# Optimization experiments

Hardware: AMD Instinct MI355X
Metric: run time of the kernel (lower is better)

Reference implementation:

```python
import jax, jax.numpy as jnp
import numpy as np

N_NODES = 100000


def gcn_conv(x, edge_index, W, b):
    """PyG GCNConv: add self-loops, symmetric D^-1/2 (A+I) D^-1/2 normalization,
    linear transform, bias. Transform-then-aggregate (out_dim <= in_dim here)."""
    src, dst = edge_index[0], edge_index[1]
    h = x @ W  # [N, out]
    # degree including self-loop (edge_weight = 1)
    ones = jnp.ones(src.shape[0], dtype=x.dtype)
    deg = jax.ops.segment_sum(ones, dst, num_segments=N_NODES) + 1.0
    dinv = jax.lax.rsqrt(deg)  # [N]
    # normalized messages over real edges
    norm = dinv[src] * dinv[dst]  # [E]
    msgs = h[src] * norm[:, None]  # [E, out] -- dominant memory traffic
    agg = jax.ops.segment_sum(msgs, dst, num_segments=N_NODES)
    # self-loop contribution: norm_ii = dinv[i]^2
    agg = agg + h * (dinv * dinv)[:, None]
    return agg + b


def setup_inputs() -> dict:
    key = jax.random.key(0)
    k1, k2, k3, k4, k5, k6 = jax.random.split(key, 6)
    in_dim, hidden_dim, out_dim = 128, 64, 32
    n_edges = 1_600_000
    x = jax.random.normal(k1, (N_NODES, in_dim), dtype=jnp.float32)
    edge_index = jax.random.randint(k2, (2, n_edges), 0, N_NODES, dtype=jnp.int64)
    s1 = 1.0 / np.sqrt(in_dim)
    s2 = 1.0 / np.sqrt(hidden_dim)
    W1 = jax.random.uniform(k3, (in_dim, hidden_dim), jnp.float32, -s1, s1)
    b1 = jax.random.uniform(k4, (hidden_dim,), jnp.float32, -s1, s1)
    W2 = jax.random.uniform(k5, (hidden_dim, out_dim), jnp.float32, -s2, s2)
    b2 = jax.random.uniform(k6, (out_dim,), jnp.float32, -s2, s2)
    return {"x": x, "edge_index": edge_index, "W1": W1, "b1": b1, "W2": W2, "b2": b2}


def reference(x, edge_index, W1, b1, W2, b2):
    h = jax.nn.relu(gcn_conv(x, edge_index, W1, b1))
    return gcn_conv(h, edge_index, W2, b2)
```

## Files before the change

### kernel.cpp

```cpp
#include <hip/hip_runtime.h>

#define N_NODES 100000

__device__ __forceinline__ unsigned short f2bf_rn(float f) {
    unsigned int b = __float_as_uint(f);
    b += 0x7fffu + ((b >> 16) & 1u);
    return (unsigned short)(b >> 16);
}
__device__ __forceinline__ float bf_lo(unsigned int u) { return __uint_as_float(u << 16); }
__device__ __forceinline__ float bf_hi(unsigned int u) { return __uint_as_float(u & 0xffff0000u); }

__global__ __launch_bounds__(256) void bcount_kernel(const int* __restrict__ dst, int E,
                                                     unsigned int* __restrict__ bucket_totals) {
    __shared__ unsigned int cnt[256];
    int t = threadIdx.x;
    cnt[t] = 0;
    __syncthreads();
    int base = blockIdx.x * 4096;
#pragma unroll
    for (int k = 0; k < 16; ++k) {
        int e = base + k * 256 + t;
        if (e < E) {
            int d = __builtin_nontemporal_load(&dst[e]);
            atomicAdd(&cnt[(unsigned int)d >> 9], 1u);
        }
    }
    __syncthreads();
    if (cnt[t] > 0) atomicAdd(&bucket_totals[t], cnt[t]);
}

__global__ __launch_bounds__(256) void bscan_kernel(const unsigned int* __restrict__ totals,
                                                    int nb, int E,
                                                    unsigned int* __restrict__ bucket_base,
                                                    unsigned int* __restrict__ bucket_cursor) {
    __shared__ unsigned int s[256];
    int t = threadIdx.x;
    unsigned int v = (t < nb) ? totals[t] : 0u;
    s[t] = v; __syncthreads();
    for (int off = 1; off < 256; off <<= 1) {
        unsigned int x = s[t];
        unsigned int y = (t >= off) ? s[t - off] : 0u;
        __syncthreads();
        s[t] = x + y;
        __syncthreads();
    }
    if (t < nb) {
        unsigned int excl = s[t] - v;
        bucket_base[t] = excl;
        bucket_cursor[t] = excl;
    }
    if (t == 0) bucket_base[nb] = (unsigned int)E;
}

__global__ __launch_bounds__(256) void bin_kernel(const int* __restrict__ ei, int E,
                                                  unsigned int* __restrict__ bucket_cursor,
                                                  unsigned int* __restrict__ binned) {
    __shared__ unsigned int cnt[256];
    __shared__ unsigned int cur[256];
    int t = threadIdx.x;
    cnt[t] = 0;
    __syncthreads();
    int base = blockIdx.x * 4096;
    unsigned int pk[16];
    unsigned int bk[16];
#pragma unroll
    for (int k = 0; k < 16; ++k) {
        int e = base + k * 256 + t;
        if (e < E) {
            int s = __builtin_nontemporal_load(&ei[e]);
            int d = __builtin_nontemporal_load(&ei[E + e]);
            unsigned int b = (unsigned int)d >> 9;
            pk[k] = (unsigned int)s | (((unsigned int)d & 511u) << 17);
            bk[k] = b;
            atomicAdd(&cnt[b], 1u);
        } else {
            bk[k] = 0xFFFFFFFFu;
        }
    }
    __syncthreads();
    if (cnt[t] > 0) cur[t] = atomicAdd(&bucket_cursor[t], cnt[t]);
    __syncthreads();
#pragma unroll
    for (int k = 0; k < 16; ++k) {
        if (bk[k] != 0xFFFFFFFFu) {
            unsigned int pos = atomicAdd(&cur[bk[k]], 1u);
            binned[pos] = pk[k];
        }
    }
}

__global__ __launch_bounds__(512) void degb_kernel(const unsigned int* __restrict__ binned,
                                                   const unsigned int* __restrict__ bucket_base,
                                                   unsigned int* __restrict__ deg,
                                                   float* __restrict__ dinv, int N) {
    __shared__ unsigned int cnt[512];
    int t = threadIdx.x;
    cnt[t] = 0;
    int beg = (int)bucket_base[blockIdx.x];
    int end = (int)bucket_base[blockIdx.x + 1];
    __syncthreads();
    for (int i = beg + t; i < end; i += 512) {
        unsigned int u = __builtin_nontemporal_load(&binned[i]);
        atomicAdd(&cnt[u >> 17], 1u);
    }
    __syncthreads();
    int node = (blockIdx.x << 9) + t;
    if (node < N) {
        unsigned int c = cnt[t];
        deg[node] = c;
        dinv[node] = rsqrtf((float)c + 1.0f);
    }
}


__global__ __launch_bounds__(256) void scanA_kernel(const unsigned int* __restrict__ deg,
                                                    int n, unsigned int* __restrict__ totals) {
    __shared__ unsigned int s[256];
    int t = threadIdx.x;
    int base = blockIdx.x * 1024 + t * 4;
    unsigned int sum = 0;
#pragma unroll
    for (int k = 0; k < 4; ++k) { int i = base + k; if (i < n) sum += deg[i]; }
    s[t] = sum; __syncthreads();
    for (int off = 128; off > 0; off >>= 1) {
        if (t < off) s[t] += s[t + off];
        __syncthreads();
    }
    if (t == 0) totals[blockIdx.x] = s[0];
}

__global__ __launch_bounds__(128) void scanB_kernel(const unsigned int* __restrict__ totals,
                                                    int nblk, unsigned int* __restrict__ offsets,
                                                    int* __restrict__ row_start, int n, int E) {
    __shared__ unsigned int s[128];
    int t = threadIdx.x;
    unsigned int v = (t < nblk) ? totals[t] : 0u;
    s[t] = v; __syncthreads();
    for (int off = 1; off < 128; off <<= 1) {
        unsigned int x = s[t];
        unsigned int y = (t >= off) ? s[t - off] : 0u;
        __syncthreads();
        s[t] = x + y;
        __syncthreads();
    }
    if (t < nblk) offsets[t] = s[t] - v;
    if (t == 0) row_start[n] = E;
}

__global__ __launch_bounds__(256) void scanC_kernel(const unsigned int* __restrict__ deg,
                                                    const unsigned int* __restrict__ offsets,
                                                    int n, int* __restrict__ row_start) {
    __shared__ unsigned int s[256];
    int t = threadIdx.x;
    int base = blockIdx.x * 1024 + t * 4;
    unsigned int v[4];
    unsigned int sum = 0;
#pragma unroll
    for (int k = 0; k < 4; ++k) { int i = base + k; v[k] = (i < n) ? deg[i] : 0u; sum += v[k]; }
    s[t] = sum; __syncthreads();
    for (int off = 1; off < 256; off <<= 1) {
        unsigned int x = s[t];
        unsigned int y = (t >= off) ? s[t - off] : 0u;
        __syncthreads();
        s[t] = x + y;
        __syncthreads();
    }
    unsigned int excl = s[t] - sum + offsets[blockIdx.x];
#pragma unroll
    for (int k = 0; k < 4; ++k) {
        int i = base + k;
        if (i < n) row_start[i] = (int)excl;
        excl += v[k];
    }
}

__global__ __launch_bounds__(1024) void place_kernel(const unsigned int* __restrict__ binned,
                                                     const int* __restrict__ row_start,
                                                     int* __restrict__ srcs, int N) {
    __shared__ int cur[512];
    int t = threadIdx.x;
    int node0 = blockIdx.x << 9;
    if (t < 512) {
        int idx = node0 + t;
        cur[t] = row_start[idx < N ? idx : N];
    }
    int endn = node0 + 512; if (endn > N) endn = N;
    int beg = row_start[node0];
    int end = row_start[endn];
    __syncthreads();
    for (int i = beg + t; i < end; i += 1024) {
        unsigned int u = __builtin_nontemporal_load(&binned[i]);
        int doff = (int)(u >> 17);
        int slot = atomicAdd(&cur[doff], 1);
        srcs[slot] = (int)(u & 0x1FFFFu);
    }
}

__global__ __launch_bounds__(256) void gemm1_kernel(
    const float* __restrict__ x, const float* __restrict__ W,
    const float* __restrict__ dinv,
    unsigned short* __restrict__ h1b, int N) {
    __shared__ float4 Ws4[128 * 16];
    __shared__ float4 xs4[64 * 33];
    int tid = threadIdx.x;
    const float4* W4 = (const float4*)W;
#pragma unroll
    for (int i = 0; i < 8; ++i) Ws4[tid + 256 * i] = W4[tid + 256 * i];
    int row0 = blockIdx.x * 64;
    const float4* x4 = (const float4*)x;
#pragma unroll
    for (int i = 0; i < 8; ++i) {
        int idx = tid + 256 * i;
        int r = idx >> 5, c = idx & 31;
        int gr = row0 + r;
        float4 v;
        if (gr < N) v = x4[(size_t)gr * 32 + c];
        else { v.x = v.y = v.z = v.w = 0.f; }
        xs4[r * 33 + c] = v;
    }
    __syncthreads();
    int tc = tid & 15;
    int tr = tid >> 4;
    float4 acc[4];
#pragma unroll
    for (int rr = 0; rr < 4; ++rr) { acc[rr].x = 0.f; acc[rr].y = 0.f; acc[rr].z = 0.f; acc[rr].w = 0.f; }
#pragma unroll 2
    for (int k4 = 0; k4 < 32; ++k4) {
        float4 xr[4], w[4];
#pragma unroll
        for (int rr = 0; rr < 4; ++rr) xr[rr] = xs4[(tr * 4 + rr) * 33 + k4];
#pragma unroll
        for (int kk = 0; kk < 4; ++kk) w[kk] = Ws4[(k4 * 4 + kk) * 16 + tc];
#pragma unroll
        for (int rr = 0; rr < 4; ++rr) {
            acc[rr].x += xr[rr].x * w[0].x; acc[rr].y += xr[rr].x * w[0].y;
            acc[rr].z += xr[rr].x * w[0].z; acc[rr].w += xr[rr].x * w[0].w;
            acc[rr].x += xr[rr].y * w[1].x; acc[rr].y += xr[rr].y * w[1].y;
            acc[rr].z += xr[rr].y * w[1].z; acc[rr].w += xr[rr].y * w[1].w;
            acc[rr].x += xr[rr].z * w[2].x; acc[rr].y += xr[rr].z * w[2].y;
            acc[rr].z += xr[rr].z * w[2].z; acc[rr].w += xr[rr].z * w[2].w;
            acc[rr].x += xr[rr].w * w[3].x; acc[rr].y += xr[rr].w * w[3].y;
            acc[rr].z += xr[rr].w * w[3].z; acc[rr].w += xr[rr].w * w[3].w;
        }
    }
#pragma unroll
    for (int rr = 0; rr < 4; ++rr) {
        int r = row0 + tr * 4 + rr;
        if (r < N) {
            float di = dinv[r];
            ushort4 o;
            o.x = f2bf_rn(acc[rr].x * di); o.y = f2bf_rn(acc[rr].y * di);
            o.z = f2bf_rn(acc[rr].z * di); o.w = f2bf_rn(acc[rr].w * di);
            *(ushort4*)(h1b + (size_t)r * 64 + tc * 4) = o;
        }
    }
}

__global__ __launch_bounds__(256) void agg1_kernel(
    const unsigned int* __restrict__ h1u,
    const int* __restrict__ srcs,
    const int* __restrict__ row_start, const float* __restrict__ dinv,
    const float* __restrict__ b1, const float* __restrict__ W2,
    unsigned short* __restrict__ h2b, int N) {
    __shared__ float W2s[64 * 32];
    __shared__ float hr[8][64];
    int tid = threadIdx.x;
    const float4* W24 = (const float4*)W2;
    float4* W2s4 = (float4*)W2s;
#pragma unroll
    for (int i = 0; i < 2; ++i) W2s4[tid + 256 * i] = W24[tid + 256 * i];
    __syncthreads();
    int nib = tid >> 5;
    int jp = tid & 31;
    int d = blockIdx.x * 8 + nib;
    if (d >= N) return;
    float di = dinv[d];
    float2 bias = ((const float2*)b1)[jp];
    unsigned int su = h1u[(size_t)d * 32 + jp];
    int beg = row_start[d], end = row_start[d + 1];
    float a0 = bf_lo(su);
    float a1 = bf_hi(su);
    int e = beg;
    for (; e + 16 <= end; e += 16) {
        int c[16];
#pragma unroll
        for (int k = 0; k < 16; ++k) c[k] = srcs[e + k];
        unsigned int u[16];
#pragma unroll
        for (int k = 0; k < 16; ++k) u[k] = h1u[(size_t)c[k] * 32 + jp];
#pragma unroll
        for (int k = 0; k < 16; ++k) { a0 += bf_lo(u[k]); a1 += bf_hi(u[k]); }
    }
    if (e + 8 <= end) {
        int c[8];
#pragma unroll
        for (int k = 0; k < 8; ++k) c[k] = srcs[e + k];
        unsigned int u[8];
#pragma unroll
        for (int k = 0; k < 8; ++k) u[k] = h1u[(size_t)c[k] * 32 + jp];
#pragma unroll
        for (int k = 0; k < 8; ++k) { a0 += bf_lo(u[k]); a1 += bf_hi(u[k]); }
        e += 8;
    }
    if (e + 4 <= end) {
        int c[4];
#pragma unroll
        for (int k = 0; k < 4; ++k) c[k] = srcs[e + k];
        unsigned int u[4];
#pragma unroll
        for (int k = 0; k < 4; ++k) u[k] = h1u[(size_t)c[k] * 32 + jp];
#pragma unroll
        for (int k = 0; k < 4; ++k) { a0 += bf_lo(u[k]); a1 += bf_hi(u[k]); }
        e += 4;
    }
    for (; e < end; ++e) {
        unsigned int u0 = h1u[(size_t)srcs[e] * 32 + jp];
        a0 += bf_lo(u0); a1 += bf_hi(u0);
    }
    float h0 = fmaxf(a0 * di + bias.x, 0.f);
    float h1v = fmaxf(a1 * di + bias.y, 0.f);
    hr[nib][2 * jp] = h0;
    hr[nib][2 * jp + 1] = h1v;
    const float* hrw = hr[nib];
    float p = 0.f;
#pragma unroll 8
    for (int k = 0; k < 64; ++k)
        p += hrw[k] * W2s[k * 32 + jp];
    h2b[(size_t)d * 32 + jp] = f2bf_rn(p * di);
}

__global__ __launch_bounds__(256) void agg2_kernel(
    const unsigned int* __restrict__ h2u,
    const int* __restrict__ srcs,
    const int* __restrict__ row_start, const float* __restrict__ dinv,
    const float* __restrict__ b2, float* __restrict__ out, int N) {
    int t = blockIdx.x * 256 + threadIdx.x;
    int d = t >> 4;
    int jp = t & 15;
    if (d >= N) return;
    float di = dinv[d];
    float2 bias = ((const float2*)b2)[jp];
    unsigned int su = h2u[(size_t)d * 16 + jp];
    int beg = row_start[d], end = row_start[d + 1];
    float a0 = bf_lo(su);
    float a1 = bf_hi(su);
    int e = beg;
    for (; e + 16 <= end; e += 16) {
        int c[16];
#pragma unroll
        for (int k = 0; k < 16; ++k) c[k] = srcs[e + k];
        unsigned int u[16];
#pragma unroll
        for (int k = 0; k < 16; ++k) u[k] = h2u[(size_t)c[k] * 16 + jp];
#pragma unroll
        for (int k = 0; k < 16; ++k) { a0 += bf_lo(u[k]); a1 += bf_hi(u[k]); }
    }
    if (e + 8 <= end) {
        int c[8];
#pragma unroll
        for (int k = 0; k < 8; ++k) c[k] = srcs[e + k];
        unsigned int u[8];
#pragma unroll
        for (int k = 0; k < 8; ++k) u[k] = h2u[(size_t)c[k] * 16 + jp];
#pragma unroll
        for (int k = 0; k < 8; ++k) { a0 += bf_lo(u[k]); a1 += bf_hi(u[k]); }
        e += 8;
    }
    if (e + 4 <= end) {
        int c[4];
#pragma unroll
        for (int k = 0; k < 4; ++k) c[k] = srcs[e + k];
        unsigned int u[4];
#pragma unroll
        for (int k = 0; k < 4; ++k) u[k] = h2u[(size_t)c[k] * 16 + jp];
#pragma unroll
        for (int k = 0; k < 4; ++k) { a0 += bf_lo(u[k]); a1 += bf_hi(u[k]); }
        e += 4;
    }
    for (; e < end; ++e) {
        unsigned int u0 = h2u[(size_t)srcs[e] * 16 + jp];
        a0 += bf_lo(u0); a1 += bf_hi(u0);
    }
    float2 r;
    r.x = a0 * di + bias.x;
    r.y = a1 * di + bias.y;
    ((float2*)(out + (size_t)d * 32))[jp] = r;
}

extern "C" void kernel_launch(void* const* d_in, const int* in_sizes, int n_in,
                              void* d_out, int out_size, void* d_ws, size_t ws_size,
                              hipStream_t stream) {
    const float* x  = (const float*)d_in[0];
    const int*   ei = (const int*)d_in[1];
    const float* W1 = (const float*)d_in[2];
    const float* b1 = (const float*)d_in[3];
    const float* W2 = (const float*)d_in[4];
    const float* b2 = (const float*)d_in[5];
    float* out = (float*)d_out;

    const int N = N_NODES;
    const int E = in_sizes[1] / 2;
    const int NBLK = (N + 1023) / 1024;
    const int NB = (N + 511) / 512;
    const int EB = (E + 4095) / 4096;

    char* p = (char*)d_ws;
    int* srcs = (int*)p;                      p += (size_t)E * 4;
    unsigned int* binned = (unsigned int*)p;  p += (size_t)E * 4;
    unsigned short* h1b = (unsigned short*)p; p += (size_t)N * 64 * 2;
    unsigned short* h2b = (unsigned short*)p; p += (size_t)N * 32 * 2;
    unsigned int* deg = (unsigned int*)p;     p += (size_t)N * 4;
    float* dinv = (float*)p;                  p += (size_t)N * 4;
    int* row_start = (int*)p;                 p += (size_t)(N + 1) * 4;
    unsigned int* bucket_totals = (unsigned int*)p; p += 256 * 4;
    unsigned int* bucket_base = (unsigned int*)p;   p += 256 * 4;
    unsigned int* bucket_cursor = (unsigned int*)p; p += 256 * 4;
    unsigned int* totals = (unsigned int*)p;  p += 128 * 4;
    unsigned int* offsets = (unsigned int*)p;

    hipMemsetAsync(bucket_totals, 0, 256 * sizeof(unsigned int), stream);

    bcount_kernel<<<EB, 256, 0, stream>>>(ei + E, E, bucket_totals);
    bscan_kernel<<<1, 256, 0, stream>>>(bucket_totals, NB, E, bucket_base, bucket_cursor);
    bin_kernel<<<EB, 256, 0, stream>>>(ei, E, bucket_cursor, binned);
    degb_kernel<<<NB, 512, 0, stream>>>(binned, bucket_base, deg, dinv, N);
    scanA_kernel<<<NBLK, 256, 0, stream>>>(deg, N, totals);
    scanB_kernel<<<1, 128, 0, stream>>>(totals, NBLK, offsets, row_start, N, E);
    scanC_kernel<<<NBLK, 256, 0, stream>>>(deg, offsets, N, row_start);
    place_kernel<<<NB, 1024, 0, stream>>>(binned, row_start, srcs, N);

    gemm1_kernel<<<(N + 63) / 64, 256, 0, stream>>>(x, W1, dinv, h1b, N);
    agg1_kernel<<<(N + 7) / 8, 256, 0, stream>>>((const unsigned int*)h1b, srcs, row_start,
                                                 dinv, b1, W2, h2b, N);
    agg2_kernel<<<(N * 16 + 255) / 256, 256, 0, stream>>>((const unsigned int*)h2b, srcs,
                                                          row_start, dinv, b2, out, N);
}
```

Before: 269.8 us.

## Fuse degree/scan/placement into one build kernel and split edges across lanes

```diff
diff --git a/kernel.cpp b/kernel.cpp
--- a/kernel.cpp
+++ b/kernel.cpp
@@ -89,109 +89,43 @@
     }
 }
 
-__global__ __launch_bounds__(512) void degb_kernel(const unsigned int* __restrict__ binned,
-                                                   const unsigned int* __restrict__ bucket_base,
-                                                   unsigned int* __restrict__ deg,
-                                                   float* __restrict__ dinv, int N) {
+__global__ __launch_bounds__(512) void build_kernel(const unsigned int* __restrict__ binned,
+                                                    const unsigned int* __restrict__ bucket_base,
+                                                    float* __restrict__ dinv,
+                                                    int* __restrict__ row_start,
+                                                    int* __restrict__ srcs, int N, int E) {
     __shared__ unsigned int cnt[512];
+    __shared__ unsigned int sc[512];
+    __shared__ int cur[512];
     int t = threadIdx.x;
     cnt[t] = 0;
     int beg = (int)bucket_base[blockIdx.x];
     int end = (int)bucket_base[blockIdx.x + 1];
     __syncthreads();
-    for (int i = beg + t; i < end; i += 512) {
-        unsigned int u = __builtin_nontemporal_load(&binned[i]);
-        atomicAdd(&cnt[u >> 17], 1u);
-    }
-    __syncthreads();
+    for (int i = beg + t; i < end; i += 512)
+        atomicAdd(&cnt[binned[i] >> 17], 1u);
+    __syncthreads();
+    unsigned int v = cnt[t];
+    sc[t] = v; __syncthreads();
+    for (int off = 1; off < 512; off <<= 1) {
+        unsigned int x = sc[t];
+        unsigned int y = (t >= off) ? sc[t - off] : 0u;
+        __syncthreads();
+        sc[t] = x + y;
+        __syncthreads();
+    }
+    int excl = beg + (int)(sc[t] - v);
     int node = (blockIdx.x << 9) + t;
     if (node < N) {
-        unsigned int c = cnt[t];
-        deg[node] = c;
-        dinv[node] = rsqrtf((float)c + 1.0f);
-    }
-}
-
-
-__global__ __launch_bounds__(256) void scanA_kernel(const unsigned int* __restrict__ deg,
-                                                    int n, unsigned int* __restrict__ totals) {
-    __shared__ unsigned int s[256];
-    int t = threadIdx.x;
-    int base = blockIdx.x * 1024 + t * 4;
-    unsigned int sum = 0;
-#pragma unroll
-    for (int k = 0; k < 4; ++k) { int i = base + k; if (i < n) sum += deg[i]; }
-    s[t] = sum; __syncthreads();
-    for (int off = 128; off > 0; off >>= 1) {
-        if (t < off) s[t] += s[t + off];
-        __syncthreads();
-    }
-    if (t == 0) totals[blockIdx.x] = s[0];
-}
-
-__global__ __launch_bounds__(128) void scanB_kernel(const unsigned int* __restrict__ totals,
-                                                    int nblk, unsigned int* __restrict__ offsets,
-                                                    int* __restrict__ row_start, int n, int E) {
-    __shared__ unsigned int s[128];
-    int t = threadIdx.x;
-    unsigned int v = (t < nblk) ? totals[t] : 0u;
-    s[t] = v; __syncthreads();
-    for (int off = 1; off < 128; off <<= 1) {
-        unsigned int x = s[t];
-        unsigned int y = (t >= off) ? s[t - off] : 0u;
-        __syncthreads();
-        s[t] = x + y;
-        __syncthreads();
-    }
-    if (t < nblk) offsets[t] = s[t] - v;
-    if (t == 0) row_start[n] = E;
-}
-
-__global__ __launch_bounds__(256) void scanC_kernel(const unsigned int* __restrict__ deg,
-                                                    const unsigned int* __restrict__ offsets,
-                                                    int n, int* __restrict__ row_start) {
-    __shared__ unsigned int s[256];
-    int t = threadIdx.x;
-    int base = blockIdx.x * 1024 + t * 4;
-    unsigned int v[4];
-    unsigned int sum = 0;
-#pragma unroll
-    for (int k = 0; k < 4; ++k) { int i = base + k; v[k] = (i < n) ? deg[i] : 0u; sum += v[k]; }
-    s[t] = sum; __syncthreads();
-    for (int off = 1; off < 256; off <<= 1) {
-        unsigned int x = s[t];
-        unsigned int y = (t >= off) ? s[t - off] : 0u;
-        __syncthreads();
-        s[t] = x + y;
-        __syncthreads();
-    }
-    unsigned int excl = s[t] - sum + offsets[blockIdx.x];
-#pragma unroll
-    for (int k = 0; k < 4; ++k) {
-        int i = base + k;
-        if (i < n) row_start[i] = (int)excl;
-        excl += v[k];
-    }
-}
-
-__global__ __launch_bounds__(1024) void place_kernel(const unsigned int* __restrict__ binned,
-                                                     const int* __restrict__ row_start,
-                                                     int* __restrict__ srcs, int N) {
-    __shared__ int cur[512];
-    int t = threadIdx.x;
-    int node0 = blockIdx.x << 9;
-    if (t < 512) {
-        int idx = node0 + t;
-        cur[t] = row_start[idx < N ? idx : N];
-    }
-    int endn = node0 + 512; if (endn > N) endn = N;
-    int beg = row_start[node0];
-    int end = row_start[endn];
-    __syncthreads();
-    for (int i = beg + t; i < end; i += 1024) {
-        unsigned int u = __builtin_nontemporal_load(&binned[i]);
-        int doff = (int)(u >> 17);
-        int slot = atomicAdd(&cur[doff], 1);
+        row_start[node] = excl;
+        dinv[node] = rsqrtf((float)v + 1.0f);
+    }
+    cur[t] = excl;
+    if (blockIdx.x == 0 && t == 0) row_start[N] = E;
+    __syncthreads();
+    for (int i = beg + t; i < end; i += 512) {
+        unsigned int u = binned[i];
+        int slot = atomicAdd(&cur[u >> 17], 1);
         srcs[slot] = (int)(u & 0x1FFFFu);
     }
 }
@@ -263,70 +197,68 @@
     const float* __restrict__ b1, const float* __restrict__ W2,
     unsigned short* __restrict__ h2b, int N) {
     __shared__ float W2s[64 * 32];
-    __shared__ float hr[8][64];
+    __shared__ float hr[4][64];
     int tid = threadIdx.x;
     const float4* W24 = (const float4*)W2;
     float4* W2s4 = (float4*)W2s;
 #pragma unroll
     for (int i = 0; i < 2; ++i) W2s4[tid + 256 * i] = W24[tid + 256 * i];
     __syncthreads();
-    int nib = tid >> 5;
-    int jp = tid & 31;
-    int d = blockIdx.x * 8 + nib;
+    int wid = tid >> 6, lane = tid & 63;
+    int eg = lane >> 5;
+    int jp = lane & 31;
+    int d = blockIdx.x * 4 + wid;
     if (d >= N) return;
     float di = dinv[d];
     float2 bias = ((const float2*)b1)[jp];
     unsigned int su = h1u[(size_t)d * 32 + jp];
     int beg = row_start[d], end = row_start[d + 1];
-    float a0 = bf_lo(su);
-    float a1 = bf_hi(su);
-    int e = beg;
-    for (; e + 16 <= end; e += 16) {
-        int c[16];
-#pragma unroll
-        for (int k = 0; k < 16; ++k) c[k] = srcs[e + k];
-        unsigned int u[16];
-#pragma unroll
-        for (int k = 0; k < 16; ++k) u[k] = h1u[(size_t)c[k] * 32 + jp];
-#pragma unroll
-        for (int k = 0; k < 16; ++k) { a0 += bf_lo(u[k]); a1 += bf_hi(u[k]); }
-    }
-    if (e + 8 <= end) {
-        int c[8];
-#pragma unroll
-        for (int k = 0; k < 8; ++k) c[k] = srcs[e + k];
-        unsigned int u[8];
+    int m = end - beg;
+    float a0 = 0.f, a1 = 0.f;
+    int e = beg + eg;
+    int nb = m >> 4;
+    for (int j = 0; j < nb; ++j) {
+        int c[8]; unsigned int u[8];
+#pragma unroll
+        for (int k = 0; k < 8; ++k) c[k] = srcs[e + 2 * k];
 #pragma unroll
         for (int k = 0; k < 8; ++k) u[k] = h1u[(size_t)c[k] * 32 + jp];
 #pragma unroll
         for (int k = 0; k < 8; ++k) { a0 += bf_lo(u[k]); a1 += bf_hi(u[k]); }
+        e += 16;
+    }
+    if (m & 8) {
+        int c[4]; unsigned int u[4];
+#pragma unroll
+        for (int k = 0; k < 4; ++k) c[k] = srcs[e + 2 * k];
+#pragma unroll
+        for (int k = 0; k < 4; ++k) u[k] = h1u[(size_t)c[k] * 32 + jp];
+#pragma unroll
+        for (int k = 0; k < 4; ++k) { a0 += bf_lo(u[k]); a1 += bf_hi(u[k]); }
         e += 8;
     }
-    if (e + 4 <= end) {
-        int c[4];
-#pragma unroll
-        for (int k = 0; k < 4; ++k) c[k] = srcs[e + k];
-        unsigned int u[4];
-#pragma unroll
-        for (int k = 0; k < 4; ++k) u[k] = h1u[(size_t)c[k] * 32 + jp];
-#pragma unroll
-        for (int k = 0; k < 4; ++k) { a0 += bf_lo(u[k]); a1 += bf_hi(u[k]); }
-        e += 4;
-    }
-    for (; e < end; ++e) {
+    for (; e < end; e += 2) {
         unsigned int u0 = h1u[(size_t)srcs[e] * 32 + jp];
         a0 += bf_lo(u0); a1 += bf_hi(u0);
     }
+    a0 += __shfl_xor(a0, 32);
+    a1 += __shfl_xor(a1, 32);
+    a0 += bf_lo(su);
+    a1 += bf_hi(su);
     float h0 = fmaxf(a0 * di + bias.x, 0.f);
     float h1v = fmaxf(a1 * di + bias.y, 0.f);
-    hr[nib][2 * jp] = h0;
-    hr[nib][2 * jp + 1] = h1v;
-    const float* hrw = hr[nib];
+    if (eg == 0) {
+        hr[wid][2 * jp] = h0;
+        hr[wid][2 * jp + 1] = h1v;
+    }
+    const float* hrw = hr[wid];
+    int k0 = eg * 32;
     float p = 0.f;
 #pragma unroll 8
-    for (int k = 0; k < 64; ++k)
-        p += hrw[k] * W2s[k * 32 + jp];
-    h2b[(size_t)d * 32 + jp] = f2bf_rn(p * di);
+    for (int k = 0; k < 32; ++k)
+        p += hrw[k0 + k] * W2s[(k0 + k) * 32 + jp];
+    p += __shfl_xor(p, 32);
+    if (eg == 0) h2b[(size_t)d * 32 + jp] = f2bf_rn(p * di);
 }
 
 __global__ __launch_bounds__(256) void agg2_kernel(
@@ -334,57 +266,50 @@
     const int* __restrict__ srcs,
     const int* __restrict__ row_start, const float* __restrict__ dinv,
     const float* __restrict__ b2, float* __restrict__ out, int N) {
-    int t = blockIdx.x * 256 + threadIdx.x;
-    int d = t >> 4;
-    int jp = t & 15;
+    int tid = threadIdx.x;
+    int wid = tid >> 6, lane = tid & 63;
+    int eg = lane >> 4;
+    int jp = lane & 15;
+    int d = blockIdx.x * 4 + wid;
     if (d >= N) return;
     float di = dinv[d];
     float2 bias = ((const float2*)b2)[jp];
     unsigned int su = h2u[(size_t)d * 16 + jp];
     int beg = row_start[d], end = row_start[d + 1];
-    float a0 = bf_lo(su);
-    float a1 = bf_hi(su);
-    int e = beg;
-    for (; e + 16 <= end; e += 16) {
-        int c[16];
-#pragma unroll
-        for (int k = 0; k < 16; ++k) c[k] = srcs[e + k];
-        unsigned int u[16];
-#pragma unroll
-        for (int k = 0; k < 16; ++k) u[k] = h2u[(size_t)c[k] * 16 + jp];
-#pragma unroll
-        for (int k = 0; k < 16; ++k) { a0 += bf_lo(u[k]); a1 += bf_hi(u[k]); }
-    }
-    if (e + 8 <= end) {
-        int c[8];
-#pragma unroll
-        for (int k = 0; k < 8; ++k) c[k] = srcs[e + k];
-        unsigned int u[8];
-#pragma unroll
-        for (int k = 0; k < 8; ++k) u[k] = h2u[(size_t)c[k] * 16 + jp];
-#pragma unroll
-        for (int k = 0; k < 8; ++k) { a0 += bf_lo(u[k]); a1 += bf_hi(u[k]); }
+    int m = end - beg;
+    float a0 = 0.f, a1 = 0.f;
+    int e = beg + eg;
+    int nb = m >> 4;
+    for (int j = 0; j < nb; ++j) {
+        int c[4]; unsigned int u[4];
+#pragma unroll
+        for (int k = 0; k < 4; ++k) c[k] = srcs[e + 4 * k];
+#pragma unroll
+        for (int k = 0; k < 4; ++k) u[k] = h2u[(size_t)c[k] * 16 + jp];
+#pragma unroll
+        for (int k = 0; k < 4; ++k) { a0 += bf_lo(u[k]); a1 += bf_hi(u[k]); }
+        e += 16;
+    }
+    if (m & 8) {
+        int c0 = srcs[e], c1 = srcs[e + 4];
+        unsigned int u0 = h2u[(size_t)c0 * 16 + jp];
+        unsigned int u1 = h2u[(size_t)c1 * 16 + jp];
+        a0 += bf_lo(u0) + bf_lo(u1);
+        a1 += bf_hi(u0) + bf_hi(u1);
         e += 8;
     }
-    if (e + 4 <= end) {
-        int c[4];
-#pragma unroll
-        for (int k = 0; k < 4; ++k) c[k] = srcs[e + k];
-        unsigned int u[4];
-#pragma unroll
-        for (int k = 0; k < 4; ++k) u[k] = h2u[(size_t)c[k] * 16 + jp];
-#pragma unroll
-        for (int k = 0; k < 4; ++k) { a0 += bf_lo(u[k]); a1 += bf_hi(u[k]); }
-        e += 4;
-    }
-    for (; e < end; ++e) {
+    for (; e < end; e += 4) {
         unsigned int u0 = h2u[(size_t)srcs[e] * 16 + jp];
         a0 += bf_lo(u0); a1 += bf_hi(u0);
     }
-    float2 r;
-    r.x = a0 * di + bias.x;
-    r.y = a1 * di + bias.y;
-    ((float2*)(out + (size_t)d * 32))[jp] = r;
+    a0 += __shfl_xor(a0, 16); a1 += __shfl_xor(a1, 16);
+    a0 += __shfl_xor(a0, 32); a1 += __shfl_xor(a1, 32);
+    if (lane < 16) {
+        float2 r;
+        r.x = (a0 + bf_lo(su)) * di + bias.x;
+        r.y = (a1 + bf_hi(su)) * di + bias.y;
+        ((float2*)(out + (size_t)d * 32))[jp] = r;
+    }
 }
 
 extern "C" void kernel_launch(void* const* d_in, const int* in_sizes, int n_in,
@@ -400,7 +325,6 @@
 
     const int N = N_NODES;
     const int E = in_sizes[1] / 2;
-    const int NBLK = (N + 1023) / 1024;
     const int NB = (N + 511) / 512;
     const int EB = (E + 4095) / 4096;
 
@@ -409,29 +333,22 @@
     unsigned int* binned = (unsigned int*)p;  p += (size_t)E * 4;
     unsigned short* h1b = (unsigned short*)p; p += (size_t)N * 64 * 2;
     unsigned short* h2b = (unsigned short*)p; p += (size_t)N * 32 * 2;
-    unsigned int* deg = (unsigned int*)p;     p += (size_t)N * 4;
     float* dinv = (float*)p;                  p += (size_t)N * 4;
     int* row_start = (int*)p;                 p += (size_t)(N + 1) * 4;
     unsigned int* bucket_totals = (unsigned int*)p; p += 256 * 4;
-    unsigned int* bucket_base = (unsigned int*)p;   p += 256 * 4;
-    unsigned int* bucket_cursor = (unsigned int*)p; p += 256 * 4;
-    unsigned int* totals = (unsigned int*)p;  p += 128 * 4;
-    unsigned int* offsets = (unsigned int*)p;
+    unsigned int* bucket_base = (unsigned int*)p;   p += 260 * 4;
+    unsigned int* bucket_cursor = (unsigned int*)p;
 
     hipMemsetAsync(bucket_totals, 0, 256 * sizeof(unsigned int), stream);
 
     bcount_kernel<<<EB, 256, 0, stream>>>(ei + E, E, bucket_totals);
     bscan_kernel<<<1, 256, 0, stream>>>(bucket_totals, NB, E, bucket_base, bucket_cursor);
     bin_kernel<<<EB, 256, 0, stream>>>(ei, E, bucket_cursor, binned);
-    degb_kernel<<<NB, 512, 0, stream>>>(binned, bucket_base, deg, dinv, N);
-    scanA_kernel<<<NBLK, 256, 0, stream>>>(deg, N, totals);
-    scanB_kernel<<<1, 128, 0, stream>>>(totals, NBLK, offsets, row_start, N, E);
-    scanC_kernel<<<NBLK, 256, 0, stream>>>(deg, offsets, N, row_start);
-    place_kernel<<<NB, 1024, 0, stream>>>(binned, row_start, srcs, N);
+    build_kernel<<<NB, 512, 0, stream>>>(binned, bucket_base, dinv, row_start, srcs, N, E);
 
     gemm1_kernel<<<(N + 63) / 64, 256, 0, stream>>>(x, W1, dinv, h1b, N);
-    agg1_kernel<<<(N + 7) / 8, 256, 0, stream>>>((const unsigned int*)h1b, srcs, row_start,
+    agg1_kernel<<<(N + 3) / 4, 256, 0, stream>>>((const unsigned int*)h1b, srcs, row_start,
                                                  dinv, b1, W2, h2b, N);
-    agg2_kernel<<<(N * 16 + 255) / 256, 256, 0, stream>>>((const unsigned int*)h2b, srcs,
-                                                          row_start, dinv, b2, out, N);
-}
+    agg2_kernel<<<(N + 3) / 4, 256, 0, stream>>>((const unsigned int*)h2b, srcs,
+                                                 row_start, dinv, b2, out, N);
+}
```

Result: slower. 281.5 us (+4.4%).
